# Performance work log

Hardware: AMD Instinct MI355X
Metric: run time of the kernel (lower is better)

The kernel has to match this reference:

```python
import jax, jax.numpy as jnp
import numpy as np

N = 100000
E = 1600000


def gcn_conv(x, W, b, src, dst, dinv):
    # PyG GCNConv: h = x @ W; symmetric normalization with self-loops;
    # out[i] = sum_{j->i} dinv[j]*dinv[i]*h[j] + dinv[i]^2*h[i] + b
    h = x @ W
    norm = dinv[src] * dinv[dst]                      # [E]
    msg = h[src] * norm[:, None]                      # [E, d] gather
    out = jax.ops.segment_sum(msg, dst, num_segments=N)  # scatter-add
    out = out + h * (dinv * dinv)[:, None]            # self-loop term
    return out + b


def setup_inputs() -> dict:
    key = jax.random.key(0)
    ks = jax.random.split(key, 8)
    nfeat, nhid, nclass = 128, 128, 40
    x = jax.random.normal(ks[0], (N, nfeat), dtype=jnp.float32)
    edge_index = jax.random.randint(ks[1], (2, E), 0, N, dtype=jnp.int64)
    s = 1.0 / np.sqrt(nfeat)
    W0 = jax.random.uniform(ks[2], (nfeat, nhid), jnp.float32, -s, s)
    b0 = jnp.zeros((nhid,), jnp.float32)
    W1 = jax.random.uniform(ks[3], (nhid, nhid), jnp.float32, -s, s)
    b1 = jnp.zeros((nhid,), jnp.float32)
    W2 = jax.random.uniform(ks[4], (nhid, nclass), jnp.float32, -s, s)
    b2 = jnp.zeros((nclass,), jnp.float32)
    return {"x": x, "W0": W0, "b0": b0, "W1": W1, "b1": b1,
            "W2": W2, "b2": b2, "edge_index": edge_index}


def reference(x, W0, b0, W1, b1, W2, b2, edge_index):
    src, dst = edge_index[0], edge_index[1]
    # degree (with self-loop) on destination nodes, symmetric norm
    deg = jax.ops.segment_sum(jnp.ones((E,), jnp.float32), dst, num_segments=N) + 1.0
    dinv = jax.lax.rsqrt(deg)
    h = gcn_conv(x, W0, b0, src, dst, dinv)
    h = jax.nn.relu(h)  # dropout is identity in eval mode
    h = gcn_conv(h, W1, b1, src, dst, dinv)
    h = jax.nn.relu(h)
    out = gcn_conv(h, W2, b2, src, dst, dinv)
    return out
```

## Files before the change

kernel.cpp:

```cpp
#include <hip/hip_runtime.h>
#include <hip/hip_fp16.h>


#define CAP 8192
#define NBMAX 512

typedef _Float16 f16;
typedef __attribute__((ext_vector_type(8))) _Float16 f16x8;
typedef __attribute__((ext_vector_type(4))) _Float16 f16x4;
typedef __attribute__((ext_vector_type(4))) float f32x4;

__global__ __launch_bounds__(256)
void bucket_prep_kernel(const int* __restrict__ src, const int* __restrict__ dst,
                        int E, int gP1, int NB,
                        int* __restrict__ bucket_cnt, unsigned* __restrict__ bucketbuf,
                        const float* __restrict__ W0, const float* __restrict__ W1,
                        const float* __restrict__ W2,
                        __half* __restrict__ w0t, __half* __restrict__ w1t,
                        __half* __restrict__ w2t) {
  int b = blockIdx.x;
  if (b < gP1) {
    __shared__ int hist[NBMAX];
    __shared__ int cbase[NBMAX];
    int tid = threadIdx.x;
    for (int i = tid; i < NB; i += 256) hist[i] = 0;
    __syncthreads();
    int e0 = b * 4096;
    int eend = min(e0 + 4096, E);
    for (int e = e0 + tid; e < eend; e += 256)
      atomicAdd(&hist[((unsigned)dst[e]) >> 8], 1);
    __syncthreads();
    for (int i = tid; i < NB; i += 256) {
      int h = hist[i];
      cbase[i] = h ? atomicAdd(&bucket_cnt[i], h) : 0;
    }
    __syncthreads();
    for (int i = tid; i < NB; i += 256) hist[i] = 0;
    __syncthreads();
    for (int e = e0 + tid; e < eend; e += 256) {
      int d = dst[e];
      int s = src[e];
      int bk = ((unsigned)d) >> 8;
      int idx = cbase[bk] + atomicAdd(&hist[bk], 1);
      if (idx < CAP)
        bucketbuf[(size_t)bk * CAP + idx] = (((unsigned)s) << 8) | (unsigned)(d & 255);
    }
  } else {
    int i = (b - gP1) * 256 + threadIdx.x;
    if (i < 16384) {
      int n = i >> 7, k = i & 127;
      w0t[i] = __float2half_rn(W0[k * 128 + n]);
    } else if (i < 32768) {
      int j = i - 16384;
      int n = j >> 7, k = j & 127;
      w1t[j] = __float2half_rn(W1[k * 128 + n]);
    } else if (i < 38912) {
      int j = i - 32768;
      int n = j >> 7, k = j & 127;
      w2t[j] = (n < 40) ? __float2half_rn(W2[k * 40 + n]) : __float2half_rn(0.f);
    }
  }
}

struct P2Shared {
  unsigned plist[CAP];
  int cnts[256];
  int sm[256];
};

__device__ __forceinline__
void phase2_body(const unsigned* __restrict__ bucketbuf, const int* __restrict__ bucket_cnt,
                 int* __restrict__ rowptr, float* __restrict__ dinv,
                 int* __restrict__ col, int N, int E, int NB, int b, P2Shared& sh) {
  int tid = threadIdx.x;
  int cnt_b = min(bucket_cnt[b], CAP);

  int part = 0;
  for (int i = tid; i < b; i += 256) part += bucket_cnt[i];
  sh.sm[tid] = part;
  __syncthreads();
#pragma unroll
  for (int off = 128; off > 0; off >>= 1) {
    if (tid < off) sh.sm[tid] += sh.sm[tid + off];
    __syncthreads();
  }
  int base = sh.sm[0];
  __syncthreads();

  for (int i = tid; i < cnt_b; i += 256)
    sh.plist[i] = bucketbuf[(size_t)b * CAP + i];
  sh.cnts[tid] = 0;
  __syncthreads();
  for (int i = tid; i < cnt_b; i += 256)
    atomicAdd(&sh.cnts[sh.plist[i] & 255u], 1);
  __syncthreads();

  int myc = sh.cnts[tid];
  sh.sm[tid] = myc;
  __syncthreads();
#pragma unroll
  for (int off = 1; off < 256; off <<= 1) {
    int u = (tid >= off) ? sh.sm[tid - off] : 0;
    __syncthreads();
    sh.sm[tid] += u;
    __syncthreads();
  }
  int exc = sh.sm[tid] - myc;

  int n = (b << 8) + tid;
  if (n < N) {
    rowptr[n] = base + exc;
    dinv[n] = 1.0f / sqrtf((float)myc + 1.0f);
  }
  if (b == NB - 1 && tid == 0) rowptr[N] = E;
  __syncthreads();

  sh.cnts[tid] = base + exc;
  __syncthreads();
  for (int i = tid; i < cnt_b; i += 256) {
    unsigned p = sh.plist[i];
    int pos = atomicAdd(&sh.cnts[p & 255u], 1);
    col[pos] = (int)(p >> 8);
  }
}

template <typename TIN, bool SCALE>
__device__ __forceinline__
void mfma_gemm128_body(const TIN* __restrict__ X, const __half* __restrict__ Wt,
                       const float* __restrict__ dinv, __half* __restrict__ G,
                       int nrows, int blk, f16 (*xs)[72], f16 (*ws)[72]) {
  const int tid = threadIdx.x;
  const int wave = tid >> 6;
  const int lane = tid & 63;
  const int mrow = lane & 15;
  const int kg = lane >> 4;
  const int row0 = blk * 128;

  f32x4 acc[2][8];
#pragma unroll
  for (int i = 0; i < 2; ++i)
#pragma unroll
    for (int j = 0; j < 8; ++j) acc[i][j] = (f32x4){0.f, 0.f, 0.f, 0.f};

  for (int k0 = 0; k0 < 128; k0 += 64) {
    if constexpr (sizeof(TIN) == 4) {
#pragma unroll
      for (int t = tid; t < 2048; t += 256) {
        int r = t >> 4;
        int kk = (t & 15) * 4;
        float4 v = make_float4(0.f, 0.f, 0.f, 0.f);
        if (row0 + r < nrows)
          v = *(const float4*)((const float*)X + (size_t)(row0 + r) * 128 + k0 + kk);
        f16x4 hv = {(f16)v.x, (f16)v.y, (f16)v.z, (f16)v.w};
        *(f16x4*)&xs[r][kk] = hv;
      }
    } else {
#pragma unroll
      for (int t = tid; t < 1024; t += 256) {
        int r = t >> 3;
        int kk = (t & 7) * 8;
        f16x8 v = (f16x8){0, 0, 0, 0, 0, 0, 0, 0};
        if (row0 + r < nrows)
          v = *(const f16x8*)((const f16*)X + (size_t)(row0 + r) * 128 + k0 + kk);
        *(f16x8*)&xs[r][kk] = v;
      }
    }
#pragma unroll
    for (int t = tid; t < 1024; t += 256) {
      int r = t >> 3;
      int kk = (t & 7) * 8;
      *(f16x8*)&ws[r][kk] =
          *(const f16x8*)((const f16*)Wt + (size_t)r * 128 + k0 + kk);
    }
    __syncthreads();
#pragma unroll
    for (int ks = 0; ks < 64; ks += 32) {
      f16x8 a0 = *(const f16x8*)&xs[wave * 32 + mrow][ks + kg * 8];
      f16x8 a1 = *(const f16x8*)&xs[wave * 32 + 16 + mrow][ks + kg * 8];
#pragma unroll
      for (int nt = 0; nt < 8; ++nt) {
        f16x8 b = *(const f16x8*)&ws[nt * 16 + mrow][ks + kg * 8];
        acc[0][nt] = __builtin_amdgcn_mfma_f32_16x16x32_f16(a0, b, acc[0][nt], 0, 0, 0);
        acc[1][nt] = __builtin_amdgcn_mfma_f32_16x16x32_f16(a1, b, acc[1][nt], 0, 0, 0);
      }
    }
    __syncthreads();
  }
#pragma unroll
  for (int mt = 0; mt < 2; ++mt) {
    int rbase = row0 + wave * 32 + mt * 16 + kg * 4;
#pragma unroll
    for (int i = 0; i < 4; ++i) {
      int grow = rbase + i;
      if (grow < nrows) {
        float s = SCALE ? dinv[grow] : 1.0f;
        __half* gp = G + (size_t)grow * 128 + mrow;
#pragma unroll
        for (int nt = 0; nt < 8; ++nt)
          gp[nt * 16] = __float2half_rn(s * acc[mt][nt][i]);
      }
    }
  }
}

__global__ __launch_bounds__(256)
void mfma_gemm128_kernel(const __half* __restrict__ X, const __half* __restrict__ Wt,
                         const float* __restrict__ dinv, __half* __restrict__ G,
                         int nrows) {
  __shared__ f16 xs[128][72];
  __shared__ f16 ws[128][72];
  mfma_gemm128_body<__half, true>(X, Wt, dinv, G, nrows, blockIdx.x, xs, ws);
}

__global__ __launch_bounds__(256)
void gemm128_build_kernel(const float* __restrict__ X, const __half* __restrict__ Wt,
                          __half* __restrict__ G, int nrows,
                          const unsigned* __restrict__ bucketbuf,
                          const int* __restrict__ bucket_cnt,
                          int* __restrict__ rowptr, float* __restrict__ dinv,
                          int* __restrict__ col, int N, int E, int NB) {
  __shared__ char shraw[2 * 128 * 72 * sizeof(f16)];
  if ((int)blockIdx.x < NB) {
    phase2_body(bucketbuf, bucket_cnt, rowptr, dinv, col, N, E, NB,
                blockIdx.x, *(P2Shared*)shraw);
  } else {
    f16 (*xs)[72] = (f16(*)[72])shraw;
    f16 (*ws)[72] = (f16(*)[72])(shraw + 128 * 72 * sizeof(f16));
    mfma_gemm128_body<float, false>(X, Wt, nullptr, G, nrows, blockIdx.x - NB, xs, ws);
  }
}

__global__ __launch_bounds__(256)
void mfma_gemm48_kernel(const __half* __restrict__ X, const __half* __restrict__ Wt,
                        const float* __restrict__ dinv, __half* __restrict__ G,
                        int nrows) {
  __shared__ f16 xs[128][72];
  __shared__ f16 ws[48][72];
  const int tid = threadIdx.x;
  const int wave = tid >> 6;
  const int lane = tid & 63;
  const int mrow = lane & 15;
  const int kg = lane >> 4;
  const int row0 = blockIdx.x * 128;

  f32x4 acc[2][3];
#pragma unroll
  for (int i = 0; i < 2; ++i)
#pragma unroll
    for (int j = 0; j < 3; ++j) acc[i][j] = (f32x4){0.f, 0.f, 0.f, 0.f};

  for (int k0 = 0; k0 < 128; k0 += 64) {
#pragma unroll
    for (int t = tid; t < 1024; t += 256) {
      int r = t >> 3;
      int kk = (t & 7) * 8;
      f16x8 v = (f16x8){0, 0, 0, 0, 0, 0, 0, 0};
      if (row0 + r < nrows)
        v = *(const f16x8*)((const f16*)X + (size_t)(row0 + r) * 128 + k0 + kk);
      *(f16x8*)&xs[r][kk] = v;
    }
#pragma unroll
    for (int t = tid; t < 384; t += 256) {
      int r = t >> 3;
      int kk = (t & 7) * 8;
      *(f16x8*)&ws[r][kk] =
          *(const f16x8*)((const f16*)Wt + (size_t)r * 128 + k0 + kk);
    }
    __syncthreads();
#pragma unroll
    for (int ks = 0; ks < 64; ks += 32) {
      f16x8 a0 = *(const f16x8*)&xs[wave * 32 + mrow][ks + kg * 8];
      f16x8 a1 = *(const f16x8*)&xs[wave * 32 + 16 + mrow][ks + kg * 8];
#pragma unroll
      for (int nt = 0; nt < 3; ++nt) {
        f16x8 b = *(const f16x8*)&ws[nt * 16 + mrow][ks + kg * 8];
        acc[0][nt] = __builtin_amdgcn_mfma_f32_16x16x32_f16(a0, b, acc[0][nt], 0, 0, 0);
        acc[1][nt] = __builtin_amdgcn_mfma_f32_16x16x32_f16(a1, b, acc[1][nt], 0, 0, 0);
      }
    }
    __syncthreads();
  }
#pragma unroll
  for (int mt = 0; mt < 2; ++mt) {
    int rbase = row0 + wave * 32 + mt * 16 + kg * 4;
#pragma unroll
    for (int i = 0; i < 4; ++i) {
      int grow = rbase + i;
      if (grow < nrows) {
        float s = dinv[grow];
#pragma unroll
        for (int nt = 0; nt < 3; ++nt) {
          int c = nt * 16 + mrow;
          if (c < 40)
            G[(size_t)grow * 64 + c] = __float2half_rn(s * acc[mt][nt][i]);
        }
      }
    }
  }
}

template <bool RELU, bool WEIGHTED, typename TOUT>
__global__ __launch_bounds__(256)
void aggregate128_kernel(const __half* __restrict__ G, const int* __restrict__ rowptr,
                         const int* __restrict__ col, const float* __restrict__ dinv,
                         const float* __restrict__ bias, TOUT* __restrict__ out,
                         int n) {
  constexpr int NPW = 4;
  int wid = threadIdx.x >> 6;
  int lane = threadIdx.x & 63;
  int n0 = (blockIdx.x * 4 + wid) * NPW;
  if (n0 >= n) return;

  int sub = lane >> 4;
  int c = lane & 15;
  const float4* g4 = (const float4*)G;

  int eA = rowptr[n0], endA = rowptr[n0 + 1];
  int n1 = min(n0 + 1, n - 1);
  int eB = rowptr[n1], endB = rowptr[n1 + 1];

  int lastA = (endA > eA) ? endA - 1 : 0;
  int iA = eA + sub;
  int cA0 = col[min(iA,      lastA)];
  int cA1 = col[min(iA + 4,  lastA)];
  int cA2 = col[min(iA + 8,  lastA)];
  int cA3 = col[min(iA + 12, lastA)];
  int cA4 = col[min(iA + 16, lastA)];

#pragma unroll
  for (int j = 0; j < NPW; ++j) {
    int node = n0 + j;
    if (node >= n) break;

    float4 r0 = g4[(size_t)cA0 * 16 + c];
    float4 r1 = g4[(size_t)cA1 * 16 + c];
    float4 r2 = g4[(size_t)cA2 * 16 + c];
    float4 r3 = g4[(size_t)cA3 * 16 + c];
    float4 r4 = g4[(size_t)cA4 * 16 + c];
    float4 rs = g4[(size_t)node * 16 + c];
    float dv0 = 1.f, dv1 = 1.f, dv2 = 1.f, dv3 = 1.f, dv4 = 1.f;
    if (WEIGHTED) {
      dv0 = dinv[cA0]; dv1 = dinv[cA1]; dv2 = dinv[cA2];
      dv3 = dinv[cA3]; dv4 = dinv[cA4];
    }
    float di = dinv[node];

    int n2 = min(node + 2, n - 1);
    int eC = rowptr[n2];
    int endC = rowptr[n2 + 1];

    int lastB = (endB > eB) ? endB - 1 : 0;
    int iB = eB + sub;
    int cB0 = col[min(iB,      lastB)];
    int cB1 = col[min(iB + 4,  lastB)];
    int cB2 = col[min(iB + 8,  lastB)];
    int cB3 = col[min(iB + 12, lastB)];
    int cB4 = col[min(iB + 16, lastB)];

    float a0 = 0.f, a1 = 0.f, a2 = 0.f, a3 = 0.f,
          a4 = 0.f, a5 = 0.f, a6 = 0.f, a7 = 0.f;
    auto accumw = [&](float4 raw, float w) {
      const __half2* h = (const __half2*)&raw;
      float2 f0 = __half22float2(h[0]);
      float2 f1 = __half22float2(h[1]);
      float2 f2 = __half22float2(h[2]);
      float2 f3 = __half22float2(h[3]);
      a0 = fmaf(w, f0.x, a0); a1 = fmaf(w, f0.y, a1);
      a2 = fmaf(w, f1.x, a2); a3 = fmaf(w, f1.y, a3);
      a4 = fmaf(w, f2.x, a4); a5 = fmaf(w, f2.y, a5);
      a6 = fmaf(w, f3.x, a6); a7 = fmaf(w, f3.y, a7);
    };
    accumw(rs, (sub == 0) ? (WEIGHTED ? di : 1.f) : 0.f);
    accumw(r0, (iA      < endA) ? dv0 : 0.f);
    accumw(r1, (iA + 4  < endA) ? dv1 : 0.f);
    accumw(r2, (iA + 8  < endA) ? dv2 : 0.f);
    accumw(r3, (iA + 12 < endA) ? dv3 : 0.f);
    accumw(r4, (iA + 16 < endA) ? dv4 : 0.f);

    for (int t = eA + 20; t < endA; t += 4) {
      int it = t + sub;
      if (it < endA) {
        int sc = col[it];
        accumw(g4[(size_t)sc * 16 + c], WEIGHTED ? dinv[sc] : 1.f);
      }
    }

    a0 += __shfl_xor(a0, 16); a1 += __shfl_xor(a1, 16);
    a2 += __shfl_xor(a2, 16); a3 += __shfl_xor(a3, 16);
    a4 += __shfl_xor(a4, 16); a5 += __shfl_xor(a5, 16);
    a6 += __shfl_xor(a6, 16); a7 += __shfl_xor(a7, 16);
    a0 += __shfl_xor(a0, 32); a1 += __shfl_xor(a1, 32);
    a2 += __shfl_xor(a2, 32); a3 += __shfl_xor(a3, 32);
    a4 += __shfl_xor(a4, 32); a5 += __shfl_xor(a5, 32);
    a6 += __shfl_xor(a6, 32); a7 += __shfl_xor(a7, 32);

    if (sub == 0) {
      const float4* b4 = (const float4*)bias;
      float4 bb0 = b4[c * 2];
      float4 bb1 = b4[c * 2 + 1];
      float o[8] = {di * a0 + bb0.x, di * a1 + bb0.y, di * a2 + bb0.z,
                    di * a3 + bb0.w, di * a4 + bb1.x, di * a5 + bb1.y,
                    di * a6 + bb1.z, di * a7 + bb1.w};
      if (RELU) {
#pragma unroll
        for (int k = 0; k < 8; ++k) o[k] = fmaxf(o[k], 0.f);
      }
      if constexpr (sizeof(TOUT) == 2) {
        union { __half2 h[4]; float4 f; } u;
        u.h[0] = __floats2half2_rn(o[0], o[1]);
        u.h[1] = __floats2half2_rn(o[2], o[3]);
        u.h[2] = __floats2half2_rn(o[4], o[5]);
        u.h[3] = __floats2half2_rn(o[6], o[7]);
        *(float4*)((__half*)out + (size_t)node * 128 + c * 8) = u.f;
      } else {
        float4* op = (float4*)((float*)out + (size_t)node * 128 + c * 8);
        op[0] = make_float4(o[0], o[1], o[2], o[3]);
        op[1] = make_float4(o[4], o[5], o[6], o[7]);
      }
    }

    eA = eB; endA = endB; eB = eC; endB = endC;
    iA = eA + sub;
    cA0 = cB0; cA1 = cB1; cA2 = cB2; cA3 = cB3; cA4 = cB4;
  }
}

__global__ __launch_bounds__(256)
void aggregate40_kernel(const __half* __restrict__ G, const int* __restrict__ rowptr,
                        const int* __restrict__ col, const float* __restrict__ dinv,
                        const float* __restrict__ bias, float* __restrict__ out,
                        int n) {
  constexpr int NPW = 4;
  int wid = threadIdx.x >> 6;
  int lane = threadIdx.x & 63;
  int n0 = (blockIdx.x * 4 + wid) * NPW;
  if (n0 >= n) return;

  int sub = lane / 10;
  int c = lane % 10;
  bool act = sub < 6;
  const float2* g2 = (const float2*)G;

  int eA = rowptr[n0], endA = rowptr[n0 + 1];
  int n1 = min(n0 + 1, n - 1);
  int eB = rowptr[n1], endB = rowptr[n1 + 1];

  int lastA = (endA > eA) ? endA - 1 : 0;
  int iA = eA + sub * 4;
  int cA0 = col[min(iA,     lastA)];
  int cA1 = col[min(iA + 1, lastA)];
  int cA2 = col[min(iA + 2, lastA)];
  int cA3 = col[min(iA + 3, lastA)];

#pragma unroll
  for (int j = 0; j < NPW; ++j) {
    int node = n0 + j;
    if (node >= n) break;

    float2 r0 = g2[(size_t)cA0 * 16 + c];
    float2 r1 = g2[(size_t)cA1 * 16 + c];
    float2 r2 = g2[(size_t)cA2 * 16 + c];
    float2 r3 = g2[(size_t)cA3 * 16 + c];
    float2 rs = g2[(size_t)node * 16 + c];
    float di = dinv[node];

    int n2 = min(node + 2, n - 1);
    int eC = rowptr[n2];
    int endC = rowptr[n2 + 1];

    int lastB = (endB > eB) ? endB - 1 : 0;
    int iB = eB + sub * 4;
    int cB0 = col[min(iB,     lastB)];
    int cB1 = col[min(iB + 1, lastB)];
    int cB2 = col[min(iB + 2, lastB)];
    int cB3 = col[min(iB + 3, lastB)];

    float ax = 0.f, ay = 0.f, az = 0.f, aw = 0.f;
    auto acc2w = [&](float2 raw, float w) {
      float2 f0 = __half22float2(*(const __half2*)&raw.x);
      float2 f1 = __half22float2(*(const __half2*)&raw.y);
      ax = fmaf(w, f0.x, ax); ay = fmaf(w, f0.y, ay);
      az = fmaf(w, f1.x, az); aw = fmaf(w, f1.y, aw);
    };
    acc2w(rs, (lane < 10) ? 1.f : 0.f);
    acc2w(r0, (act && iA     < endA) ? 1.f : 0.f);
    acc2w(r1, (act && iA + 1 < endA) ? 1.f : 0.f);
    acc2w(r2, (act && iA + 2 < endA) ? 1.f : 0.f);
    acc2w(r3, (act && iA + 3 < endA) ? 1.f : 0.f);

    for (int t = eA + 24; t < endA; t += 6) {
      int it = t + sub;
      if (act && it < endA) {
        int sc = col[it];
        acc2w(g2[(size_t)sc * 16 + c], 1.f);
      }
    }

    float bx = __shfl(ax, lane + 30), by = __shfl(ay, lane + 30),
          bz = __shfl(az, lane + 30), bw = __shfl(aw, lane + 30);
    ax += bx; ay += by; az += bz; aw += bw;
    float c1x = __shfl(ax, lane + 10), c1y = __shfl(ay, lane + 10),
          c1z = __shfl(az, lane + 10), c1w = __shfl(aw, lane + 10);
    float c2x = __shfl(ax, lane + 20), c2y = __shfl(ay, lane + 20),
          c2z = __shfl(az, lane + 20), c2w = __shfl(aw, lane + 20);

    if (lane < 10) {
      float sx = ax + c1x + c2x;
      float sy = ay + c1y + c2y;
      float sz = az + c1z + c2z;
      float sw = aw + c1w + c2w;
      float4 bb = ((const float4*)bias)[c];
      float4 o = make_float4(di * sx + bb.x, di * sy + bb.y, di * sz + bb.z,
                             di * sw + bb.w);
      ((float4*)out)[(size_t)node * 10 + c] = o;
    }

    eA = eB; endA = endB; eB = eC; endB = endC;
    iA = eA + sub * 4;
    cA0 = cB0; cA1 = cB1; cA2 = cB2; cA3 = cB3;
  }
}

extern "C" void kernel_launch(void* const* d_in, const int* in_sizes, int n_in,
                              void* d_out, int out_size, void* d_ws, size_t ws_size,
                              hipStream_t stream) {
  const float* x = (const float*)d_in[0];
  const float* W0 = (const float*)d_in[1];
  const float* b0 = (const float*)d_in[2];
  const float* W1 = (const float*)d_in[3];
  const float* b1 = (const float*)d_in[4];
  const float* W2 = (const float*)d_in[5];
  const float* b2 = (const float*)d_in[6];
  const int* ei = (const int*)d_in[7];

  const int N = in_sizes[0] / 128;
  const int E = in_sizes[7] / 2;
  const int* src = ei;
  const int* dst = ei + E;
  const int NB = (N + 255) >> 8;

  char* w = (char*)d_ws;
  size_t off = 0;
  auto alloc = [&](size_t bytes) -> void* {
    void* p = w + off;
    off = (off + bytes + 255) & ~(size_t)255;
    return p;
  };
  int* bucket_cnt = (int*)alloc((size_t)NBMAX * 4);
  float* dinv = (float*)alloc((size_t)N * 4);
  int* rowptr = (int*)alloc((size_t)(N + 1) * 4);
  int* col = (int*)alloc((size_t)E * 4);
  unsigned* bucketbuf = (unsigned*)alloc((size_t)NB * CAP * 4);
  __half* gbuf = (__half*)alloc((size_t)N * 128 * 2);
  __half* hbuf = (__half*)alloc((size_t)N * 128 * 2);
  __half* w0t = (__half*)alloc(128 * 128 * 2);
  __half* w1t = (__half*)alloc(128 * 128 * 2);
  __half* w2t = (__half*)alloc(48 * 128 * 2);
  (void)ws_size;

  hipMemsetAsync(bucket_cnt, 0, (size_t)NBMAX * 4, stream);

  dim3 blk(256);
  int gP1 = (E + 4095) / 4096;
  int gW = (38912 + 255) / 256;
  int gGemm = (N + 127) / 128;
  int gAgg = (N + 15) / 16;

  bucket_prep_kernel<<<gP1 + gW, blk, 0, stream>>>(src, dst, E, gP1, NB,
                                                   bucket_cnt, bucketbuf,
                                                   W0, W1, W2, w0t, w1t, w2t);
  gemm128_build_kernel<<<gGemm + NB, blk, 0, stream>>>(x, w0t, gbuf, N,
                                                       bucketbuf, bucket_cnt,
                                                       rowptr, dinv, col, N, E, NB);

  aggregate128_kernel<true, true, __half><<<gAgg, blk, 0, stream>>>(
      gbuf, rowptr, col, dinv, b0, hbuf, N);
  mfma_gemm128_kernel<<<gGemm, blk, 0, stream>>>(hbuf, w1t, dinv, gbuf, N);
  aggregate128_kernel<true, false, __half><<<gAgg, blk, 0, stream>>>(
      gbuf, rowptr, col, dinv, b1, hbuf, N);
  mfma_gemm48_kernel<<<gGemm, blk, 0, stream>>>(hbuf, w2t, dinv, gbuf, N);
  aggregate40_kernel<<<gAgg, blk, 0, stream>>>(gbuf, rowptr, col, dinv, b2,
                                               (float*)d_out, N);
}
```

Before: 342.6 us.

## Fuse neighbor aggregation with following layer GEMM via shared-memory tile

Measured after the change: 337.1 us. Within noise of the previous version (-1.6%).

```diff
diff --git a/kernel.cpp b/kernel.cpp
--- a/kernel.cpp
+++ b/kernel.cpp
@@ -201,15 +201,6 @@
       }
     }
   }
-}
-
-__global__ __launch_bounds__(256)
-void mfma_gemm128_kernel(const __half* __restrict__ X, const __half* __restrict__ Wt,
-                         const float* __restrict__ dinv, __half* __restrict__ G,
-                         int nrows) {
-  __shared__ f16 xs[128][72];
-  __shared__ f16 ws[128][72];
-  mfma_gemm128_body<__half, true>(X, Wt, dinv, G, nrows, blockIdx.x, xs, ws);
 }
 
 __global__ __launch_bounds__(256)
@@ -230,94 +221,27 @@
   }
 }
 
-__global__ __launch_bounds__(256)
-void mfma_gemm48_kernel(const __half* __restrict__ X, const __half* __restrict__ Wt,
-                        const float* __restrict__ dinv, __half* __restrict__ G,
-                        int nrows) {
-  __shared__ f16 xs[128][72];
-  __shared__ f16 ws[48][72];
+template <bool WEIGHTED, int NT, int OSTR>
+__global__ __launch_bounds__(256, 4)
+void agg_gemm_kernel(const __half* __restrict__ G_in, const int* __restrict__ rowptr,
+                     const int* __restrict__ col, const float* __restrict__ dinv,
+                     const float* __restrict__ bias, const __half* __restrict__ Wt,
+                     __half* __restrict__ G_out, int n) {
+  __shared__ f16 xs[128][136];
   const int tid = threadIdx.x;
   const int wave = tid >> 6;
   const int lane = tid & 63;
-  const int mrow = lane & 15;
-  const int kg = lane >> 4;
-  const int row0 = blockIdx.x * 128;
-
-  f32x4 acc[2][3];
-#pragma unroll
-  for (int i = 0; i < 2; ++i)
-#pragma unroll
-    for (int j = 0; j < 3; ++j) acc[i][j] = (f32x4){0.f, 0.f, 0.f, 0.f};
-
-  for (int k0 = 0; k0 < 128; k0 += 64) {
-#pragma unroll
-    for (int t = tid; t < 1024; t += 256) {
-      int r = t >> 3;
-      int kk = (t & 7) * 8;
-      f16x8 v = (f16x8){0, 0, 0, 0, 0, 0, 0, 0};
-      if (row0 + r < nrows)
-        v = *(const f16x8*)((const f16*)X + (size_t)(row0 + r) * 128 + k0 + kk);
-      *(f16x8*)&xs[r][kk] = v;
-    }
-#pragma unroll
-    for (int t = tid; t < 384; t += 256) {
-      int r = t >> 3;
-      int kk = (t & 7) * 8;
-      *(f16x8*)&ws[r][kk] =
-          *(const f16x8*)((const f16*)Wt + (size_t)r * 128 + k0 + kk);
-    }
-    __syncthreads();
-#pragma unroll
-    for (int ks = 0; ks < 64; ks += 32) {
-      f16x8 a0 = *(const f16x8*)&xs[wave * 32 + mrow][ks + kg * 8];
-      f16x8 a1 = *(const f16x8*)&xs[wave * 32 + 16 + mrow][ks + kg * 8];
-#pragma unroll
-      for (int nt = 0; nt < 3; ++nt) {
-        f16x8 b = *(const f16x8*)&ws[nt * 16 + mrow][ks + kg * 8];
-        acc[0][nt] = __builtin_amdgcn_mfma_f32_16x16x32_f16(a0, b, acc[0][nt], 0, 0, 0);
-        acc[1][nt] = __builtin_amdgcn_mfma_f32_16x16x32_f16(a1, b, acc[1][nt], 0, 0, 0);
-      }
-    }
-    __syncthreads();
-  }
-#pragma unroll
-  for (int mt = 0; mt < 2; ++mt) {
-    int rbase = row0 + wave * 32 + mt * 16 + kg * 4;
-#pragma unroll
-    for (int i = 0; i < 4; ++i) {
-      int grow = rbase + i;
-      if (grow < nrows) {
-        float s = dinv[grow];
-#pragma unroll
-        for (int nt = 0; nt < 3; ++nt) {
-          int c = nt * 16 + mrow;
-          if (c < 40)
-            G[(size_t)grow * 64 + c] = __float2half_rn(s * acc[mt][nt][i]);
-        }
-      }
-    }
-  }
-}
-
-template <bool RELU, bool WEIGHTED, typename TOUT>
-__global__ __launch_bounds__(256)
-void aggregate128_kernel(const __half* __restrict__ G, const int* __restrict__ rowptr,
-                         const int* __restrict__ col, const float* __restrict__ dinv,
-                         const float* __restrict__ bias, TOUT* __restrict__ out,
-                         int n) {
-  constexpr int NPW = 4;
-  int wid = threadIdx.x >> 6;
-  int lane = threadIdx.x & 63;
-  int n0 = (blockIdx.x * 4 + wid) * NPW;
+  const int sub = lane >> 4;
+  const int c = lane & 15;
+  const float4* g4 = (const float4*)G_in;
+
+  const int nbase = blockIdx.x * 128;
+  const int n0 = nbase + wave * 32;
   if (n0 >= n) return;
 
-  int sub = lane >> 4;
-  int c = lane & 15;
-  const float4* g4 = (const float4*)G;
-
   int eA = rowptr[n0], endA = rowptr[n0 + 1];
-  int n1 = min(n0 + 1, n - 1);
-  int eB = rowptr[n1], endB = rowptr[n1 + 1];
+  int nn1 = min(n0 + 1, n - 1);
+  int eB = rowptr[nn1], endB = rowptr[nn1 + 1];
 
   int lastA = (endA > eA) ? endA - 1 : 0;
   int iA = eA + sub;
@@ -327,8 +251,7 @@
   int cA3 = col[min(iA + 12, lastA)];
   int cA4 = col[min(iA + 16, lastA)];
 
-#pragma unroll
-  for (int j = 0; j < NPW; ++j) {
+  for (int j = 0; j < 32; ++j) {
     int node = n0 + j;
     if (node >= n) break;
 
@@ -398,30 +321,61 @@
       const float4* b4 = (const float4*)bias;
       float4 bb0 = b4[c * 2];
       float4 bb1 = b4[c * 2 + 1];
-      float o[8] = {di * a0 + bb0.x, di * a1 + bb0.y, di * a2 + bb0.z,
-                    di * a3 + bb0.w, di * a4 + bb1.x, di * a5 + bb1.y,
-                    di * a6 + bb1.z, di * a7 + bb1.w};
-      if (RELU) {
-#pragma unroll
-        for (int k = 0; k < 8; ++k) o[k] = fmaxf(o[k], 0.f);
-      }
-      if constexpr (sizeof(TOUT) == 2) {
-        union { __half2 h[4]; float4 f; } u;
-        u.h[0] = __floats2half2_rn(o[0], o[1]);
-        u.h[1] = __floats2half2_rn(o[2], o[3]);
-        u.h[2] = __floats2half2_rn(o[4], o[5]);
-        u.h[3] = __floats2half2_rn(o[6], o[7]);
-        *(float4*)((__half*)out + (size_t)node * 128 + c * 8) = u.f;
-      } else {
-        float4* op = (float4*)((float*)out + (size_t)node * 128 + c * 8);
-        op[0] = make_float4(o[0], o[1], o[2], o[3]);
-        op[1] = make_float4(o[4], o[5], o[6], o[7]);
-      }
+      float o0 = fmaxf(di * a0 + bb0.x, 0.f);
+      float o1 = fmaxf(di * a1 + bb0.y, 0.f);
+      float o2 = fmaxf(di * a2 + bb0.z, 0.f);
+      float o3 = fmaxf(di * a3 + bb0.w, 0.f);
+      float o4 = fmaxf(di * a4 + bb1.x, 0.f);
+      float o5 = fmaxf(di * a5 + bb1.y, 0.f);
+      float o6 = fmaxf(di * a6 + bb1.z, 0.f);
+      float o7 = fmaxf(di * a7 + bb1.w, 0.f);
+      f16x8 hv = {(f16)o0, (f16)o1, (f16)o2, (f16)o3,
+                  (f16)o4, (f16)o5, (f16)o6, (f16)o7};
+      *(f16x8*)&xs[wave * 32 + j][c * 8] = hv;
     }
 
     eA = eB; endA = endB; eB = eC; endB = endC;
     iA = eA + sub;
     cA0 = cB0; cA1 = cB1; cA2 = cB2; cA3 = cB3; cA4 = cB4;
+  }
+
+  const int mrow = c;
+  const int kg = sub;
+  f32x4 acc[2][NT];
+#pragma unroll
+  for (int i = 0; i < 2; ++i)
+#pragma unroll
+    for (int j = 0; j < NT; ++j) acc[i][j] = (f32x4){0.f, 0.f, 0.f, 0.f};
+
+#pragma unroll
+  for (int ks = 0; ks < 128; ks += 32) {
+    f16x8 fa0 = *(const f16x8*)&xs[wave * 32 + mrow][ks + kg * 8];
+    f16x8 fa1 = *(const f16x8*)&xs[wave * 32 + 16 + mrow][ks + kg * 8];
+#pragma unroll
+    for (int nt = 0; nt < NT; ++nt) {
+      f16x8 b = *(const f16x8*)((const f16*)Wt +
+                                (size_t)(nt * 16 + mrow) * 128 + ks + kg * 8);
+      acc[0][nt] = __builtin_amdgcn_mfma_f32_16x16x32_f16(fa0, b, acc[0][nt], 0, 0, 0);
+      acc[1][nt] = __builtin_amdgcn_mfma_f32_16x16x32_f16(fa1, b, acc[1][nt], 0, 0, 0);
+    }
+  }
+
+#pragma unroll
+  for (int mt = 0; mt < 2; ++mt) {
+    int rbase = n0 + mt * 16 + kg * 4;
+#pragma unroll
+    for (int i = 0; i < 4; ++i) {
+      int grow = rbase + i;
+      if (grow < n) {
+        float s = dinv[grow];
+        __half* gp = G_out + (size_t)grow * OSTR + mrow;
+#pragma unroll
+        for (int nt = 0; nt < NT; ++nt) {
+          if (OSTR == 128 || nt * 16 + mrow < 40)
+            gp[nt * 16] = __float2half_rn(s * acc[mt][nt][i]);
+        }
+      }
+    }
   }
 }
 
@@ -573,12 +527,11 @@
                                                        bucketbuf, bucket_cnt,
                                                        rowptr, dinv, col, N, E, NB);
 
-  aggregate128_kernel<true, true, __half><<<gAgg, blk, 0, stream>>>(
-      gbuf, rowptr, col, dinv, b0, hbuf, N);
-  mfma_gemm128_kernel<<<gGemm, blk, 0, stream>>>(hbuf, w1t, dinv, gbuf, N);
-  aggregate128_kernel<true, false, __half><<<gAgg, blk, 0, stream>>>(
-      gbuf, rowptr, col, dinv, b1, hbuf, N);
-  mfma_gemm48_kernel<<<gGemm, blk, 0, stream>>>(hbuf, w2t, dinv, gbuf, N);
+  agg_gemm_kernel<true, 8, 128><<<gGemm, blk, 0, stream>>>(
+      gbuf, rowptr, col, dinv, b0, w1t, hbuf, N);
+  agg_gemm_kernel<false, 3, 64><<<gGemm, blk, 0, stream>>>(
+      hbuf, rowptr, col, dinv, b1, w2t, gbuf, N);
+
   aggregate40_kernel<<<gAgg, blk, 0, stream>>>(gbuf, rowptr, col, dinv, b2,
                                                (float*)d_out, N);
 }
```

## Fuse layer-1 aggregation with layer-2 GEMM via shared-memory tile

Applied to the files above, without the earlier changes.

Measured after the change: 339.6 us. Within noise of the previous version (-0.9%).

```diff
diff --git a/kernel.cpp b/kernel.cpp
--- a/kernel.cpp
+++ b/kernel.cpp
@@ -201,15 +201,6 @@
       }
     }
   }
-}
-
-__global__ __launch_bounds__(256)
-void mfma_gemm128_kernel(const __half* __restrict__ X, const __half* __restrict__ Wt,
-                         const float* __restrict__ dinv, __half* __restrict__ G,
-                         int nrows) {
-  __shared__ f16 xs[128][72];
-  __shared__ f16 ws[128][72];
-  mfma_gemm128_body<__half, true>(X, Wt, dinv, G, nrows, blockIdx.x, xs, ws);
 }
 
 __global__ __launch_bounds__(256)
@@ -299,25 +290,27 @@
   }
 }
 
-template <bool RELU, bool WEIGHTED, typename TOUT>
-__global__ __launch_bounds__(256)
-void aggregate128_kernel(const __half* __restrict__ G, const int* __restrict__ rowptr,
-                         const int* __restrict__ col, const float* __restrict__ dinv,
-                         const float* __restrict__ bias, TOUT* __restrict__ out,
-                         int n) {
-  constexpr int NPW = 4;
-  int wid = threadIdx.x >> 6;
-  int lane = threadIdx.x & 63;
-  int n0 = (blockIdx.x * 4 + wid) * NPW;
+template <bool WEIGHTED, int NT, int OSTR>
+__global__ __launch_bounds__(256, 4)
+void agg_gemm_kernel(const __half* __restrict__ G_in, const int* __restrict__ rowptr,
+                     const int* __restrict__ col, const float* __restrict__ dinv,
+                     const float* __restrict__ bias, const __half* __restrict__ Wt,
+                     __half* __restrict__ G_out, int n) {
+  __shared__ f16 xs[128][136];
+  const int tid = threadIdx.x;
+  const int wave = tid >> 6;
+  const int lane = tid & 63;
+  const int sub = lane >> 4;
+  const int c = lane & 15;
+  const float4* g4 = (const float4*)G_in;
+
+  const int nbase = blockIdx.x * 128;
+  const int n0 = nbase + wave * 32;
   if (n0 >= n) return;
 
-  int sub = lane >> 4;
-  int c = lane & 15;
-  const float4* g4 = (const float4*)G;
-
   int eA = rowptr[n0], endA = rowptr[n0 + 1];
-  int n1 = min(n0 + 1, n - 1);
-  int eB = rowptr[n1], endB = rowptr[n1 + 1];
+  int nn1 = min(n0 + 1, n - 1);
+  int eB = rowptr[nn1], endB = rowptr[nn1 + 1];
 
   int lastA = (endA > eA) ? endA - 1 : 0;
   int iA = eA + sub;
@@ -327,8 +320,7 @@
   int cA3 = col[min(iA + 12, lastA)];
   int cA4 = col[min(iA + 16, lastA)];
 
-#pragma unroll
-  for (int j = 0; j < NPW; ++j) {
+  for (int j = 0; j < 32; ++j) {
     int node = n0 + j;
     if (node >= n) break;
 
@@ -398,6 +390,163 @@
       const float4* b4 = (const float4*)bias;
       float4 bb0 = b4[c * 2];
       float4 bb1 = b4[c * 2 + 1];
+      float o0 = fmaxf(di * a0 + bb0.x, 0.f);
+      float o1 = fmaxf(di * a1 + bb0.y, 0.f);
+      float o2 = fmaxf(di * a2 + bb0.z, 0.f);
+      float o3 = fmaxf(di * a3 + bb0.w, 0.f);
+      float o4 = fmaxf(di * a4 + bb1.x, 0.f);
+      float o5 = fmaxf(di * a5 + bb1.y, 0.f);
+      float o6 = fmaxf(di * a6 + bb1.z, 0.f);
+      float o7 = fmaxf(di * a7 + bb1.w, 0.f);
+      f16x8 hv = {(f16)o0, (f16)o1, (f16)o2, (f16)o3,
+                  (f16)o4, (f16)o5, (f16)o6, (f16)o7};
+      *(f16x8*)&xs[wave * 32 + j][c * 8] = hv;
+    }
+
+    eA = eB; endA = endB; eB = eC; endB = endC;
+    iA = eA + sub;
+    cA0 = cB0; cA1 = cB1; cA2 = cB2; cA3 = cB3; cA4 = cB4;
+  }
+
+  const int mrow = c;
+  const int kg = sub;
+  f32x4 acc[2][NT];
+#pragma unroll
+  for (int i = 0; i < 2; ++i)
+#pragma unroll
+    for (int j = 0; j < NT; ++j) acc[i][j] = (f32x4){0.f, 0.f, 0.f, 0.f};
+
+#pragma unroll
+  for (int ks = 0; ks < 128; ks += 32) {
+    f16x8 fa0 = *(const f16x8*)&xs[wave * 32 + mrow][ks + kg * 8];
+    f16x8 fa1 = *(const f16x8*)&xs[wave * 32 + 16 + mrow][ks + kg * 8];
+#pragma unroll
+    for (int nt = 0; nt < NT; ++nt) {
+      f16x8 b = *(const f16x8*)((const f16*)Wt +
+                                (size_t)(nt * 16 + mrow) * 128 + ks + kg * 8);
+      acc[0][nt] = __builtin_amdgcn_mfma_f32_16x16x32_f16(fa0, b, acc[0][nt], 0, 0, 0);
+      acc[1][nt] = __builtin_amdgcn_mfma_f32_16x16x32_f16(fa1, b, acc[1][nt], 0, 0, 0);
+    }
+  }
+
+#pragma unroll
+  for (int mt = 0; mt < 2; ++mt) {
+    int rbase = n0 + mt * 16 + kg * 4;
+#pragma unroll
+    for (int i = 0; i < 4; ++i) {
+      int grow = rbase + i;
+      if (grow < n) {
+        float s = dinv[grow];
+        __half* gp = G_out + (size_t)grow * OSTR + mrow;
+#pragma unroll
+        for (int nt = 0; nt < NT; ++nt) {
+          if (OSTR == 128 || nt * 16 + mrow < 40)
+            gp[nt * 16] = __float2half_rn(s * acc[mt][nt][i]);
+        }
+      }
+    }
+  }
+}
+
+template <bool RELU, bool WEIGHTED, typename TOUT>
+__global__ __launch_bounds__(256)
+void aggregate128_kernel(const __half* __restrict__ G, const int* __restrict__ rowptr,
+                         const int* __restrict__ col, const float* __restrict__ dinv,
+                         const float* __restrict__ bias, TOUT* __restrict__ out,
+                         int n) {
+  constexpr int NPW = 4;
+  int wid = threadIdx.x >> 6;
+  int lane = threadIdx.x & 63;
+  int n0 = (blockIdx.x * 4 + wid) * NPW;
+  if (n0 >= n) return;
+
+  int sub = lane >> 4;
+  int c = lane & 15;
+  const float4* g4 = (const float4*)G;
+
+  int eA = rowptr[n0], endA = rowptr[n0 + 1];
+  int n1 = min(n0 + 1, n - 1);
+  int eB = rowptr[n1], endB = rowptr[n1 + 1];
+
+  int lastA = (endA > eA) ? endA - 1 : 0;
+  int iA = eA + sub;
+  int cA0 = col[min(iA,      lastA)];
+  int cA1 = col[min(iA + 4,  lastA)];
+  int cA2 = col[min(iA + 8,  lastA)];
+  int cA3 = col[min(iA + 12, lastA)];
+  int cA4 = col[min(iA + 16, lastA)];
+
+#pragma unroll
+  for (int j = 0; j < NPW; ++j) {
+    int node = n0 + j;
+    if (node >= n) break;
+
+    float4 r0 = g4[(size_t)cA0 * 16 + c];
+    float4 r1 = g4[(size_t)cA1 * 16 + c];
+    float4 r2 = g4[(size_t)cA2 * 16 + c];
+    float4 r3 = g4[(size_t)cA3 * 16 + c];
+    float4 r4 = g4[(size_t)cA4 * 16 + c];
+    float4 rs = g4[(size_t)node * 16 + c];
+    float dv0 = 1.f, dv1 = 1.f, dv2 = 1.f, dv3 = 1.f, dv4 = 1.f;
+    if (WEIGHTED) {
+      dv0 = dinv[cA0]; dv1 = dinv[cA1]; dv2 = dinv[cA2];
+      dv3 = dinv[cA3]; dv4 = dinv[cA4];
+    }
+    float di = dinv[node];
+
+    int n2 = min(node + 2, n - 1);
+    int eC = rowptr[n2];
+    int endC = rowptr[n2 + 1];
+
+    int lastB = (endB > eB) ? endB - 1 : 0;
+    int iB = eB + sub;
+    int cB0 = col[min(iB,      lastB)];
+    int cB1 = col[min(iB + 4,  lastB)];
+    int cB2 = col[min(iB + 8,  lastB)];
+    int cB3 = col[min(iB + 12, lastB)];
+    int cB4 = col[min(iB + 16, lastB)];
+
+    float a0 = 0.f, a1 = 0.f, a2 = 0.f, a3 = 0.f,
+          a4 = 0.f, a5 = 0.f, a6 = 0.f, a7 = 0.f;
+    auto accumw = [&](float4 raw, float w) {
+      const __half2* h = (const __half2*)&raw;
+      float2 f0 = __half22float2(h[0]);
+      float2 f1 = __half22float2(h[1]);
+      float2 f2 = __half22float2(h[2]);
+      float2 f3 = __half22float2(h[3]);
+      a0 = fmaf(w, f0.x, a0); a1 = fmaf(w, f0.y, a1);
+      a2 = fmaf(w, f1.x, a2); a3 = fmaf(w, f1.y, a3);
+      a4 = fmaf(w, f2.x, a4); a5 = fmaf(w, f2.y, a5);
+      a6 = fmaf(w, f3.x, a6); a7 = fmaf(w, f3.y, a7);
+    };
+    accumw(rs, (sub == 0) ? (WEIGHTED ? di : 1.f) : 0.f);
+    accumw(r0, (iA      < endA) ? dv0 : 0.f);
+    accumw(r1, (iA + 4  < endA) ? dv1 : 0.f);
+    accumw(r2, (iA + 8  < endA) ? dv2 : 0.f);
+    accumw(r3, (iA + 12 < endA) ? dv3 : 0.f);
+    accumw(r4, (iA + 16 < endA) ? dv4 : 0.f);
+
+    for (int t = eA + 20; t < endA; t += 4) {
+      int it = t + sub;
+      if (it < endA) {
+        int sc = col[it];
+        accumw(g4[(size_t)sc * 16 + c], WEIGHTED ? dinv[sc] : 1.f);
+      }
+    }
+
+    a0 += __shfl_xor(a0, 16); a1 += __shfl_xor(a1, 16);
+    a2 += __shfl_xor(a2, 16); a3 += __shfl_xor(a3, 16);
+    a4 += __shfl_xor(a4, 16); a5 += __shfl_xor(a5, 16);
+    a6 += __shfl_xor(a6, 16); a7 += __shfl_xor(a7, 16);
+    a0 += __shfl_xor(a0, 32); a1 += __shfl_xor(a1, 32);
+    a2 += __shfl_xor(a2, 32); a3 += __shfl_xor(a3, 32);
+    a4 += __shfl_xor(a4, 32); a5 += __shfl_xor(a5, 32);
+    a6 += __shfl_xor(a6, 32); a7 += __shfl_xor(a7, 32);
+
+    if (sub == 0) {
+      const float4* b4 = (const float4*)bias;
+      float4 bb0 = b4[c * 2];
+      float4 bb1 = b4[c * 2 + 1];
       float o[8] = {di * a0 + bb0.x, di * a1 + bb0.y, di * a2 + bb0.z,
                     di * a3 + bb0.w, di * a4 + bb1.x, di * a5 + bb1.y,
                     di * a6 + bb1.z, di * a7 + bb1.w};
@@ -573,12 +722,13 @@
                                                        bucketbuf, bucket_cnt,
                                                        rowptr, dinv, col, N, E, NB);
 
-  aggregate128_kernel<true, true, __half><<<gAgg, blk, 0, stream>>>(
-      gbuf, rowptr, col, dinv, b0, hbuf, N);
-  mfma_gemm128_kernel<<<gGemm, blk, 0, stream>>>(hbuf, w1t, dinv, gbuf, N);
+  agg_gemm_kernel<true, 8, 128><<<gGemm, blk, 0, stream>>>(
+      gbuf, rowptr, col, dinv, b0, w1t, hbuf, N);
+
   aggregate128_kernel<true, false, __half><<<gAgg, blk, 0, stream>>>(
-      gbuf, rowptr, col, dinv, b1, hbuf, N);
-  mfma_gemm48_kernel<<<gGemm, blk, 0, stream>>>(hbuf, w2t, dinv, gbuf, N);
-  aggregate40_kernel<<<gAgg, blk, 0, stream>>>(gbuf, rowptr, col, dinv, b2,
+      hbuf, rowptr, col, dinv, b1, gbuf, N);
+  mfma_gemm48_kernel<<<gGemm, blk, 0, stream>>>(gbuf, w2t, dinv, hbuf, N);
+
+  aggregate40_kernel<<<gAgg, blk, 0, stream>>>(hbuf, rowptr, col, dinv, b2,
                                                (float*)d_out, N);
 }
```
